# Kernel optimization log

Hardware: AMD Instinct MI355X
Metric: run time of the kernel (lower is better)

Reference implementation:

```python
import jax, jax.numpy as jnp
import numpy as np

H = 1024       # hidden_size
NH = 16        # num_heads
HD = H // NH   # head_dim
I = 4096       # intermediate_size
EPS = 1e-6


def setup_inputs() -> dict:
    key = jax.random.key(0)
    ks = jax.random.split(key, 10)
    s = 0.02
    return {
        "hidden_states": jax.random.normal(ks[0], (8, 1025, H), jnp.float32),
        "qkv_w": jax.random.normal(ks[1], (3 * H, H), jnp.float32) * s,
        "qkv_b": jnp.zeros((3 * H,), jnp.float32),
        "proj_w": jax.random.normal(ks[2], (H, H), jnp.float32) * s,
        "proj_b": jnp.zeros((H,), jnp.float32),
        "fc1_w": jax.random.normal(ks[3], (I, H), jnp.float32) * s,
        "fc1_b": jnp.zeros((I,), jnp.float32),
        "fc2_w": jax.random.normal(ks[4], (H, I), jnp.float32) * s,
        "fc2_b": jnp.zeros((H,), jnp.float32),
        "norm1_w": jnp.ones((H,), jnp.float32),
        "norm1_b": jnp.zeros((H,), jnp.float32),
        "norm2_w": jnp.ones((H,), jnp.float32),
        "norm2_b": jnp.zeros((H,), jnp.float32),
        "ls1": jnp.ones((H,), jnp.float32),
        "ls2": jnp.ones((H,), jnp.float32),
    }


def _layer_norm(x, w, b):
    mu = jnp.mean(x, axis=-1, keepdims=True)
    var = jnp.mean(jnp.square(x - mu), axis=-1, keepdims=True)
    return (x - mu) * jax.lax.rsqrt(var + EPS) * w + b


def _attention(x, qkv_w, qkv_b, proj_w, proj_b):
    B, N, _ = x.shape
    qkv = x @ qkv_w.T + qkv_b                       # [B,N,3H]
    qkv = qkv.reshape(B, N, 3, NH, HD)
    q, k, v = qkv[:, :, 0], qkv[:, :, 1], qkv[:, :, 2]  # [B,N,NH,HD]
    scale = HD ** -0.5
    scores = jnp.einsum("bqhd,bkhd->bhqk", q, k) * scale
    attn = jax.nn.softmax(scores, axis=-1)
    out = jnp.einsum("bhqk,bkhd->bqhd", attn, v).reshape(B, N, H)
    return out @ proj_w.T + proj_b


def _mlp(x, fc1_w, fc1_b, fc2_w, fc2_b):
    h = jax.nn.gelu(x @ fc1_w.T + fc1_b, approximate=False)
    return h @ fc2_w.T + fc2_b


def reference(hidden_states, qkv_w, qkv_b, proj_w, proj_b, fc1_w, fc1_b,
              fc2_w, fc2_b, norm1_w, norm1_b, norm2_w, norm2_b, ls1, ls2):
    x = hidden_states
    x = x + ls1 * _attention(_layer_norm(x, norm1_w, norm1_b),
                             qkv_w, qkv_b, proj_w, proj_b)
    x = x + ls2 * _mlp(_layer_norm(x, norm2_w, norm2_b),
                       fc1_w, fc1_b, fc2_w, fc2_b)
    return x
```

## Files before the change

### kernel.cpp

```cpp
#include <hip/hip_runtime.h>
#include <cstdint>
#include <cstddef>

typedef __bf16 bf16;
typedef __bf16 bf16x8 __attribute__((ext_vector_type(8)));
typedef __bf16 bf16x4 __attribute__((ext_vector_type(4)));
typedef float  floatx4 __attribute__((ext_vector_type(4)));

#define MFMA16(a,b,c) __builtin_amdgcn_mfma_f32_16x16x32_bf16((a),(b),(c),0,0,0)

__device__ __forceinline__ void async_copy16(void* lds, const void* g) {
    __builtin_amdgcn_global_load_lds(
        (const __attribute__((address_space(1))) unsigned int*)g,
        (__attribute__((address_space(3))) unsigned int*)lds,
        16, 0, 0);
}

__global__ __launch_bounds__(256) void cvt_all(const float* __restrict__ s0,
                                               const float* __restrict__ s1,
                                               const float* __restrict__ s2,
                                               const float* __restrict__ s3,
                                               bf16* __restrict__ d0,
                                               bf16* __restrict__ d1,
                                               bf16* __restrict__ d2,
                                               bf16* __restrict__ d3) {
    const int blk = blockIdx.x;
    const float* src; bf16* dst; int base;
    if (blk < 3072)      { src = s0; dst = d0; base = blk; }
    else if (blk < 4096) { src = s1; dst = d1; base = blk - 3072; }
    else if (blk < 8192) { src = s2; dst = d2; base = blk - 4096; }
    else                 { src = s3; dst = d3; base = blk - 8192; }
    const int i = base * 256 + threadIdx.x;
    const float4 v = ((const float4*)src)[i];
    bf16x4 o;
    o[0] = (bf16)v.x; o[1] = (bf16)v.y; o[2] = (bf16)v.z; o[3] = (bf16)v.w;
    ((bf16x4*)dst)[i] = o;
}

__global__ __launch_bounds__(256) void ln_kernel(const float* __restrict__ x,
                                                 const float* __restrict__ w,
                                                 const float* __restrict__ b,
                                                 bf16* __restrict__ out) {
    const int row = blockIdx.x;
    const int t = threadIdx.x;
    const float4 v = ((const float4*)(x + (size_t)row * 1024))[t];
    float s  = v.x + v.y + v.z + v.w;
    float ss = v.x*v.x + v.y*v.y + v.z*v.z + v.w*v.w;
#pragma unroll
    for (int m = 32; m >= 1; m >>= 1) {
        s  += __shfl_xor(s,  m, 64);
        ss += __shfl_xor(ss, m, 64);
    }
    __shared__ float red[8];
    const int wave = t >> 6, lane = t & 63;
    if (lane == 0) { red[wave] = s; red[4 + wave] = ss; }
    __syncthreads();
    s  = red[0] + red[1] + red[2] + red[3];
    ss = red[4] + red[5] + red[6] + red[7];
    const float mean = s * (1.0f / 1024.0f);
    const float var  = ss * (1.0f / 1024.0f) - mean * mean;
    const float inv  = rsqrtf(var + 1e-6f);
    const float4 wv = ((const float4*)w)[t];
    const float4 bv = ((const float4*)b)[t];
    bf16x4 o;
    o[0] = (bf16)((v.x - mean) * inv * wv.x + bv.x);
    o[1] = (bf16)((v.y - mean) * inv * wv.y + bv.y);
    o[2] = (bf16)((v.z - mean) * inv * wv.z + bv.z);
    o[3] = (bf16)((v.w - mean) * inv * wv.w + bv.w);
    *(bf16x4*)(out + (size_t)row * 1024 + t * 4) = o;
}

template <int EPI, bool MSTRIP>
__global__ __launch_bounds__(256, 3) void gemm_bt(
    const bf16* __restrict__ A, const bf16* __restrict__ B,
    const float* __restrict__ bias, void* __restrict__ Cout,
    const float* __restrict__ res, const float* __restrict__ lsv,
    int M, int N, int K, int mt_per) {
    __shared__ bf16 sA[128 * 64];
    __shared__ bf16 sB[128 * 64];
    const int tid  = threadIdx.x;
    const int wave = tid >> 6;
    const int lane = tid & 63;
    const int lrow = lane & 15;
    const int quad = lane >> 4;
    int m0, n0;
    if constexpr (MSTRIP) {
        const int mtile = blockIdx.x * mt_per + blockIdx.y % mt_per;
        const int ntile = blockIdx.y / mt_per;
        m0 = mtile * 128;
        n0 = ntile * 128;
        if (m0 >= M) return;
    } else {
        const int nx   = gridDim.x;
        const int lin  = blockIdx.y * nx + blockIdx.x;
        const int w    = nx >> 3;
        const int xcd  = lin & 7;
        const int slot = lin >> 3;
        const int ntile = xcd * w + (slot % w);
        const int mtile = slot / w;
        m0 = mtile * 128;
        n0 = ntile * 128;
    }
    const int wm = (wave >> 1) * 64;
    const int wn = (wave & 1) * 64;

    floatx4 acc[4][4] = {};

    const int srow  = tid >> 3;
    const int spart = (tid & 7) ^ (srow & 7);
    const bf16* Ag[4];
    const bf16* Bg[4];
#pragma unroll
    for (int c = 0; c < 4; c++) {
        int am = m0 + c * 32 + srow; if (am > M - 1) am = M - 1;
        Ag[c] = A + (size_t)am * K + spart * 8;
        Bg[c] = B + (size_t)(n0 + c * 32 + srow) * K + spart * 8;
    }
    const int sswz = lrow & 7;

    for (int kk = 0; kk < K; kk += 64) {
        __syncthreads();
#pragma unroll
        for (int c = 0; c < 4; c++) {
            async_copy16(&sA[(c * 256 + wave * 64) * 8], Ag[c] + kk);
            async_copy16(&sB[(c * 256 + wave * 64) * 8], Bg[c] + kk);
        }
        __syncthreads();
#pragma unroll
        for (int kq = 0; kq < 2; kq++) {
            const int so = ((kq * 4 + quad) ^ sswz) * 8;
            bf16x8 af[4], bfr[4];
#pragma unroll
            for (int i = 0; i < 4; i++)
                af[i] = *(const bf16x8*)&sA[(wm + i * 16 + lrow) * 64 + so];
#pragma unroll
            for (int j = 0; j < 4; j++)
                bfr[j] = *(const bf16x8*)&sB[(wn + j * 16 + lrow) * 64 + so];
#pragma unroll
            for (int i = 0; i < 4; i++)
#pragma unroll
                for (int j = 0; j < 4; j++)
                    acc[i][j] = MFMA16(af[i], bfr[j], acc[i][j]);
        }
    }

    const int nb = n0 + wn + lrow;
#pragma unroll
    for (int i = 0; i < 4; i++) {
        const int mb = m0 + wm + i * 16 + quad * 4;
#pragma unroll
        for (int r = 0; r < 4; r++) {
            const int m = mb + r;
            if (m < M) {
#pragma unroll
                for (int j = 0; j < 4; j++) {
                    const int n = nb + j * 16;
                    float v = acc[i][j][r] + bias[n];
                    if constexpr (EPI == 0) {
                        ((bf16*)Cout)[(size_t)m * N + n] = (bf16)v;
                    } else if constexpr (EPI == 2) {
                        const float s_ = v * (0.7978845608f + 0.0356774081f * v * v);
                        const float e2s = __builtin_amdgcn_exp2f(2.8853900817779268f * s_);
                        const float g = v * (1.0f - __builtin_amdgcn_rcpf(1.0f + e2s));
                        ((bf16*)Cout)[(size_t)m * N + n] = (bf16)g;
                    } else {
                        ((float*)Cout)[(size_t)m * N + n] =
                            res[(size_t)m * N + n] + lsv[n] * v;
                    }
                }
            }
        }
    }
}

__global__ __launch_bounds__(256) void transpose_v(const bf16* __restrict__ qkv,
                                                   bf16* __restrict__ vt) {
    const int tt = blockIdx.x;
    const int bh = blockIdx.y;
    const int b = bh >> 4, h = bh & 15;
    __shared__ bf16 tile[64][72];
    const int t = threadIdx.x;
    const int tok0 = tt * 64;
#pragma unroll
    for (int i = 0; i < 4; i++) {
        const int idx4 = i * 256 + t;
        const int tl = idx4 >> 4;
        const int d4 = (idx4 & 15) * 4;
        const int tok = tok0 + tl;
        bf16x4 val;
        val[0] = (bf16)0.0f; val[1] = (bf16)0.0f; val[2] = (bf16)0.0f; val[3] = (bf16)0.0f;
        if (tok <= 1024) {
            val = *(const bf16x4*)(qkv + ((size_t)(b * 1025 + tok)) * 3072 + 2048 + h * 64 + d4);
        }
        tile[d4 + 0][tl] = val[0];
        tile[d4 + 1][tl] = val[1];
        tile[d4 + 2][tl] = val[2];
        tile[d4 + 3][tl] = val[3];
    }
    __syncthreads();
#pragma unroll
    for (int i = 0; i < 4; i++) {
        const int idx4 = i * 256 + t;
        const int d = idx4 >> 4;
        const int t4 = (idx4 & 15) * 4;
        bf16x4 o;
        o[0] = tile[d][t4 + 0]; o[1] = tile[d][t4 + 1];
        o[2] = tile[d][t4 + 2]; o[3] = tile[d][t4 + 3];
        *(bf16x4*)(vt + ((size_t)bh * 64 + d) * 1152 + tok0 + t4) = o;
    }
}

__global__ __launch_bounds__(256, 4) void attn_kernel(const bf16* __restrict__ qkv,
                                                      const bf16* __restrict__ vt,
                                                      bf16* __restrict__ o_out) {
    const int qt = blockIdx.x;
    const int bh = blockIdx.y;
    const int b = bh >> 4, h = bh & 15;
    __shared__ bf16 sK[2 * 64 * 32];
    __shared__ bf16 sV[2 * 64 * 32];
    __shared__ bf16 sQP[4 * 16 * 72];
    const int tid = threadIdx.x, wave = tid >> 6, lane = tid & 63;
    const int lrow = lane & 15, quad = lane >> 4, lko = quad * 8;
    const float cexp = 0.18033688011112042f;
    const size_t row0 = (size_t)b * 1025;

#pragma unroll
    for (int i = 0; i < 2; i++) {
        const int g = i * 256 + tid;
        const int ks = g >> 8, rr = (g >> 2) & 63, p = g & 3;
        int qrow = qt * 64 + rr; if (qrow > 1024) qrow = 1024;
        async_copy16(&sQP[(i * 256 + wave * 64) * 8],
                     qkv + (row0 + qrow) * 3072 + h * 64 + ks * 32 + p * 8);
    }
    __syncthreads();
    bf16x8 qf[2];
    qf[0] = *(const bf16x8*)&sQP[(wave * 16 + lrow) * 32 + lko];
    qf[1] = *(const bf16x8*)&sQP[2048 + (wave * 16 + lrow) * 32 + lko];
#pragma unroll
    for (int i = 0; i < 8; i++) {
        qf[0][i] = (bf16)((float)qf[0][i] * cexp);
        qf[1][i] = (bf16)((float)qf[1][i] * cexp);
    }
    bf16x8 ones;
#pragma unroll
    for (int i = 0; i < 8; i++) ones[i] = (bf16)1.0f;

    floatx4 o[4] = {};
    floatx4 ol = {};
    bf16* pw = &sQP[wave * (16 * 72)];

    for (int ktile = 0; ktile < 17; ++ktile) {
        const int kt0 = ktile * 64;
        __syncthreads();
#pragma unroll
        for (int i = 0; i < 2; i++) {
            const int g = i * 256 + tid;
            const int ks = g >> 8, tok = (g >> 2) & 63, p = g & 3;
            int krow = kt0 + tok; if (krow > 1024) krow = 1024;
            async_copy16(&sK[(i * 256 + wave * 64) * 8],
                         qkv + (row0 + krow) * 3072 + 1024 + h * 64 + ks * 32 + p * 8);
        }
#pragma unroll
        for (int i = 0; i < 2; i++) {
            const int g = i * 256 + tid;
            const int kc = g >> 8, d = (g >> 2) & 63, p = g & 3;
            async_copy16(&sV[(i * 256 + wave * 64) * 8],
                         vt + ((size_t)bh * 64 + d) * 1152 + kt0 + kc * 32 + p * 8);
        }
        __syncthreads();

        const bool lastTile = (ktile == 16);
#pragma unroll
        for (int nt = 0; nt < 4; nt++) {
            bf16x8 k0 = *(const bf16x8*)&sK[(nt * 16 + lrow) * 32 + lko];
            bf16x8 k1 = *(const bf16x8*)&sK[2048 + (nt * 16 + lrow) * 32 + lko];
            floatx4 z = {};
            z = MFMA16(k0, qf[0], z);
            z = MFMA16(k1, qf[1], z);
            bf16x4 pb;
#pragma unroll
            for (int r = 0; r < 4; r++) {
                float p = __builtin_amdgcn_exp2f(z[r]);
                if (lastTile) {
                    const int ktok = kt0 + nt * 16 + quad * 4 + r;
                    p = (ktok <= 1024) ? p : 0.0f;
                }
                pb[r] = (bf16)p;
            }
            *(bf16x4*)&pw[lrow * 72 + nt * 16 + quad * 4] = pb;
        }
#pragma unroll
        for (int ks = 0; ks < 2; ks++) {
            bf16x8 pa = *(const bf16x8*)&pw[lrow * 72 + ks * 32 + lko];
#pragma unroll
            for (int j = 0; j < 4; j++) {
                bf16x8 vb = *(const bf16x8*)&sV[ks * 2048 + (j * 16 + lrow) * 32 + lko];
                o[j] = MFMA16(pa, vb, o[j]);
            }
            ol = MFMA16(pa, ones, ol);
        }
    }

#pragma unroll
    for (int r = 0; r < 4; r++) {
        const int q = qt * 64 + wave * 16 + quad * 4 + r;
        if (q <= 1024) {
            const float inv = 1.0f / ol[r];
            const size_t orow = (row0 + q) * 1024 + h * 64;
#pragma unroll
            for (int j = 0; j < 4; j++)
                o_out[orow + j * 16 + lrow] = (bf16)(o[j][r] * inv);
        }
    }
}

extern "C" void kernel_launch(void* const* d_in, const int* in_sizes, int n_in,
                              void* d_out, int out_size, void* d_ws, size_t ws_size,
                              hipStream_t stream) {
    const float* x      = (const float*)d_in[0];
    const float* qkv_w  = (const float*)d_in[1];
    const float* qkv_b  = (const float*)d_in[2];
    const float* proj_w = (const float*)d_in[3];
    const float* proj_b = (const float*)d_in[4];
    const float* fc1_w  = (const float*)d_in[5];
    const float* fc1_b  = (const float*)d_in[6];
    const float* fc2_w  = (const float*)d_in[7];
    const float* fc2_b  = (const float*)d_in[8];
    const float* n1w    = (const float*)d_in[9];
    const float* n1b    = (const float*)d_in[10];
    const float* n2w    = (const float*)d_in[11];
    const float* n2b    = (const float*)d_in[12];
    const float* ls1    = (const float*)d_in[13];
    const float* ls2    = (const float*)d_in[14];

    char* ws = (char*)d_ws;
    bf16*  wqkv  = (bf16*)(ws + 0);
    bf16*  wproj = (bf16*)(ws + 6291456);
    bf16*  wfc1  = (bf16*)(ws + 8388608);
    bf16*  wfc2  = (bf16*)(ws + 16777216);
    bf16*  vt    = (bf16*)(ws + 25165824);
    bf16*  attnO = (bf16*)(ws + 44040192);
    float* x1    = (float*)(ws + 60833792);
    bf16*  lnbuf = (bf16*)(ws + 94420992);
    bf16*  big   = (bf16*)(ws + 111214592);

    const int M = 8200;

    cvt_all<<<12288, 256, 0, stream>>>(qkv_w, proj_w, fc1_w, fc2_w,
                                       wqkv, wproj, wfc1, wfc2);

    ln_kernel<<<M, 256, 0, stream>>>(x, n1w, n1b, lnbuf);
    gemm_bt<0, false><<<dim3(24, 65), 256, 0, stream>>>(lnbuf, wqkv, qkv_b, (void*)big,
                                                        nullptr, nullptr, M, 3072, 1024, 0);
    transpose_v<<<dim3(17, 128), 256, 0, stream>>>(big, vt);
    attn_kernel<<<dim3(17, 128), 256, 0, stream>>>(big, vt, attnO);
    gemm_bt<1, true><<<dim3(8, 72), 256, 0, stream>>>(attnO, wproj, proj_b, (void*)x1,
                                                      x, ls1, M, 1024, 1024, 9);
    ln_kernel<<<M, 256, 0, stream>>>(x1, n2w, n2b, lnbuf);
    gemm_bt<2, false><<<dim3(32, 65), 256, 0, stream>>>(lnbuf, wfc1, fc1_b, (void*)big,
                                                        nullptr, nullptr, M, 4096, 1024, 0);
    gemm_bt<3, true><<<dim3(8, 72), 256, 0, stream>>>(big, wfc2, fc2_b, d_out,
                                                      x1, ls2, M, 1024, 4096, 9);
}
```

Baseline: 505.8 us.

## Split-K the projection and fc2 GEMMs with atomic accumulation into pre-initialized output

The two N=1024 GEMMs (attention projection and fc2) are split along K into two halves via gridDim.z, doubling the number of blocks to improve occupancy across the GPU. A new init_out kernel first writes residual + ls*bias into the output, and each K-slice then atomically adds ls*partial into it. This trades extra atomic traffic and an extra elementwise pass over the output for more parallelism in the under-filled GEMMs, and makes the floating-point summation order nondeterministic.

```diff
diff --git a/kernel.cpp b/kernel.cpp
--- a/kernel.cpp
+++ b/kernel.cpp
@@ -37,6 +37,21 @@
     ((bf16x4*)dst)[i] = o;
 }
 
+__global__ __launch_bounds__(256) void init_out(const float* __restrict__ res,
+                                                const float* __restrict__ lsv,
+                                                const float* __restrict__ bias,
+                                                float* __restrict__ out) {
+    const size_t i = (size_t)blockIdx.x * 256 + threadIdx.x;
+    const int n4 = (int)(i & 255);
+    const float4 r = ((const float4*)res)[i];
+    const float4 l = ((const float4*)lsv)[n4];
+    const float4 b = ((const float4*)bias)[n4];
+    float4 o;
+    o.x = r.x + l.x * b.x; o.y = r.y + l.y * b.y;
+    o.z = r.z + l.z * b.z; o.w = r.w + l.w * b.w;
+    ((float4*)out)[i] = o;
+}
+
 __global__ __launch_bounds__(256) void ln_kernel(const float* __restrict__ x,
                                                  const float* __restrict__ w,
                                                  const float* __restrict__ b,
@@ -74,7 +89,7 @@
 __global__ __launch_bounds__(256, 3) void gemm_bt(
     const bf16* __restrict__ A, const bf16* __restrict__ B,
     const float* __restrict__ bias, void* __restrict__ Cout,
-    const float* __restrict__ res, const float* __restrict__ lsv,
+    const float* __restrict__ lsv,
     int M, int N, int K, int mt_per) {
     __shared__ bf16 sA[128 * 64];
     __shared__ bf16 sB[128 * 64];
@@ -101,6 +116,8 @@
         m0 = mtile * 128;
         n0 = ntile * 128;
     }
+    const int kLen = K / gridDim.z;
+    const int k0   = blockIdx.z * kLen;
     const int wm = (wave >> 1) * 64;
     const int wn = (wave & 1) * 64;
 
@@ -118,7 +135,7 @@
     }
     const int sswz = lrow & 7;
 
-    for (int kk = 0; kk < K; kk += 64) {
+    for (int kk = k0; kk < k0 + kLen; kk += 64) {
         __syncthreads();
 #pragma unroll
         for (int c = 0; c < 4; c++) {
@@ -155,17 +172,18 @@
 #pragma unroll
                 for (int j = 0; j < 4; j++) {
                     const int n = nb + j * 16;
-                    float v = acc[i][j][r] + bias[n];
                     if constexpr (EPI == 0) {
+                        const float v = acc[i][j][r] + bias[n];
                         ((bf16*)Cout)[(size_t)m * N + n] = (bf16)v;
                     } else if constexpr (EPI == 2) {
+                        const float v = acc[i][j][r] + bias[n];
                         const float s_ = v * (0.7978845608f + 0.0356774081f * v * v);
                         const float e2s = __builtin_amdgcn_exp2f(2.8853900817779268f * s_);
                         const float g = v * (1.0f - __builtin_amdgcn_rcpf(1.0f + e2s));
                         ((bf16*)Cout)[(size_t)m * N + n] = (bf16)g;
                     } else {
-                        ((float*)Cout)[(size_t)m * N + n] =
-                            res[(size_t)m * N + n] + lsv[n] * v;
+                        unsafeAtomicAdd(&((float*)Cout)[(size_t)m * N + n],
+                                        lsv[n] * acc[i][j][r]);
                     }
                 }
             }
@@ -351,14 +369,16 @@
 
     ln_kernel<<<M, 256, 0, stream>>>(x, n1w, n1b, lnbuf);
     gemm_bt<0, false><<<dim3(24, 65), 256, 0, stream>>>(lnbuf, wqkv, qkv_b, (void*)big,
-                                                        nullptr, nullptr, M, 3072, 1024, 0);
+                                                        nullptr, M, 3072, 1024, 0);
     transpose_v<<<dim3(17, 128), 256, 0, stream>>>(big, vt);
     attn_kernel<<<dim3(17, 128), 256, 0, stream>>>(big, vt, attnO);
-    gemm_bt<1, true><<<dim3(8, 72), 256, 0, stream>>>(attnO, wproj, proj_b, (void*)x1,
-                                                      x, ls1, M, 1024, 1024, 9);
+    init_out<<<M, 256, 0, stream>>>(x, ls1, proj_b, x1);
+    gemm_bt<1, true><<<dim3(8, 72, 2), 256, 0, stream>>>(attnO, wproj, nullptr, (void*)x1,
+                                                         ls1, M, 1024, 1024, 9);
     ln_kernel<<<M, 256, 0, stream>>>(x1, n2w, n2b, lnbuf);
     gemm_bt<2, false><<<dim3(32, 65), 256, 0, stream>>>(lnbuf, wfc1, fc1_b, (void*)big,
-                                                        nullptr, nullptr, M, 4096, 1024, 0);
-    gemm_bt<3, true><<<dim3(8, 72), 256, 0, stream>>>(big, wfc2, fc2_b, d_out,
-                                                      x1, ls2, M, 1024, 4096, 9);
-}
+                                                        nullptr, M, 4096, 1024, 0);
+    init_out<<<M, 256, 0, stream>>>(x1, ls2, fc2_b, (float*)d_out);
+    gemm_bt<1, true><<<dim3(8, 72, 2), 256, 0, stream>>>(big, wfc2, nullptr, d_out,
+                                                         ls2, M, 1024, 4096, 9);
+}
```

Result: slower. 620.1 us (+22.6%).

## Double-buffer LDS tiles in GEMM and attention to overlap loads with MFMA

Applied to the files above, without the earlier changes.

The GEMM now uses two LDS buffers with a K-step of 32 and a paired-row tile layout. The next tile is prefetched asynchronously while MFMAs run on the current one, cutting the loop to one barrier per iteration. The attention kernel gets the same treatment for its K and V tiles, with an extra barrier so the Q staging area can be reused for P. Occupancy hints are retuned (GEMM 4 blocks, attention 3) to fit the larger LDS footprint. In exchange, the GEMM has half the work per barrier and a new LDS layout that may cause bank conflicts.

```diff
diff --git a/kernel.cpp b/kernel.cpp
--- a/kernel.cpp
+++ b/kernel.cpp
@@ -71,13 +71,13 @@
 }
 
 template <int EPI, bool MSTRIP>
-__global__ __launch_bounds__(256, 3) void gemm_bt(
+__global__ __launch_bounds__(256, 4) void gemm_bt(
     const bf16* __restrict__ A, const bf16* __restrict__ B,
     const float* __restrict__ bias, void* __restrict__ Cout,
     const float* __restrict__ res, const float* __restrict__ lsv,
     int M, int N, int K, int mt_per) {
-    __shared__ bf16 sA[128 * 64];
-    __shared__ bf16 sB[128 * 64];
+    __shared__ bf16 sA[2][4096];
+    __shared__ bf16 sB[2][4096];
     const int tid  = threadIdx.x;
     const int wave = tid >> 6;
     const int lane = tid & 63;
@@ -106,42 +106,51 @@
 
     floatx4 acc[4][4] = {};
 
-    const int srow  = tid >> 3;
-    const int spart = (tid & 7) ^ (srow & 7);
-    const bf16* Ag[4];
-    const bf16* Bg[4];
-#pragma unroll
-    for (int c = 0; c < 4; c++) {
-        int am = m0 + c * 32 + srow; if (am > M - 1) am = M - 1;
-        Ag[c] = A + (size_t)am * K + spart * 8;
-        Bg[c] = B + (size_t)(n0 + c * 32 + srow) * K + spart * 8;
-    }
-    const int sswz = lrow & 7;
-
-    for (int kk = 0; kk < K; kk += 64) {
+    const int part = tid & 3;
+    int mA0 = m0 + 2 * (tid >> 3) + ((tid >> 2) & 1);
+    int mA1 = mA0 + 64;
+    if (mA0 > M - 1) mA0 = M - 1;
+    if (mA1 > M - 1) mA1 = M - 1;
+    const int nB0 = n0 + 2 * (tid >> 3) + ((tid >> 2) & 1);
+    const bf16* AgC0 = A + (size_t)mA0 * K + part * 8;
+    const bf16* AgC1 = A + (size_t)mA1 * K + part * 8;
+    const bf16* BgC0 = B + (size_t)nB0 * K + part * 8;
+    const bf16* BgC1 = B + (size_t)(nB0 + 64) * K + part * 8;
+    const int ldsOff0 = wave * 512;
+    const int ldsOff1 = 2048 + wave * 512;
+
+    const int niter = K / 32;
+    async_copy16(&sA[0][ldsOff0], AgC0);
+    async_copy16(&sA[0][ldsOff1], AgC1);
+    async_copy16(&sB[0][ldsOff0], BgC0);
+    async_copy16(&sB[0][ldsOff1], BgC1);
+
+    const int fbase = (lrow & 1) * 32 + quad * 8;
+    int cur = 0;
+    for (int it = 0; it < niter; ++it) {
         __syncthreads();
-#pragma unroll
-        for (int c = 0; c < 4; c++) {
-            async_copy16(&sA[(c * 256 + wave * 64) * 8], Ag[c] + kk);
-            async_copy16(&sB[(c * 256 + wave * 64) * 8], Bg[c] + kk);
-        }
-        __syncthreads();
-#pragma unroll
-        for (int kq = 0; kq < 2; kq++) {
-            const int so = ((kq * 4 + quad) ^ sswz) * 8;
-            bf16x8 af[4], bfr[4];
-#pragma unroll
-            for (int i = 0; i < 4; i++)
-                af[i] = *(const bf16x8*)&sA[(wm + i * 16 + lrow) * 64 + so];
+        if (it + 1 < niter) {
+            const int kk = (it + 1) * 32;
+            bf16* a = sA[cur ^ 1]; bf16* bb = sB[cur ^ 1];
+            async_copy16(&a[ldsOff0],  AgC0 + kk);
+            async_copy16(&a[ldsOff1],  AgC1 + kk);
+            async_copy16(&bb[ldsOff0], BgC0 + kk);
+            async_copy16(&bb[ldsOff1], BgC1 + kk);
+        }
+        const bf16* a = sA[cur]; const bf16* bb = sB[cur];
+        bf16x8 af[4], bfr[4];
+#pragma unroll
+        for (int i = 0; i < 4; i++)
+            af[i] = *(const bf16x8*)&a[((wm >> 1) + i * 8 + (lrow >> 1)) * 64 + fbase];
+#pragma unroll
+        for (int j = 0; j < 4; j++)
+            bfr[j] = *(const bf16x8*)&bb[((wn >> 1) + j * 8 + (lrow >> 1)) * 64 + fbase];
+#pragma unroll
+        for (int i = 0; i < 4; i++)
 #pragma unroll
             for (int j = 0; j < 4; j++)
-                bfr[j] = *(const bf16x8*)&sB[(wn + j * 16 + lrow) * 64 + so];
-#pragma unroll
-            for (int i = 0; i < 4; i++)
-#pragma unroll
-                for (int j = 0; j < 4; j++)
-                    acc[i][j] = MFMA16(af[i], bfr[j], acc[i][j]);
-        }
+                acc[i][j] = MFMA16(af[i], bfr[j], acc[i][j]);
+        cur ^= 1;
     }
 
     const int nb = n0 + wn + lrow;
@@ -155,7 +164,7 @@
 #pragma unroll
                 for (int j = 0; j < 4; j++) {
                     const int n = nb + j * 16;
-                    float v = acc[i][j][r] + bias[n];
+                    const float v = acc[i][j][r] + bias[n];
                     if constexpr (EPI == 0) {
                         ((bf16*)Cout)[(size_t)m * N + n] = (bf16)v;
                     } else if constexpr (EPI == 2) {
@@ -210,15 +219,15 @@
     }
 }
 
-__global__ __launch_bounds__(256, 4) void attn_kernel(const bf16* __restrict__ qkv,
+__global__ __launch_bounds__(256, 3) void attn_kernel(const bf16* __restrict__ qkv,
                                                       const bf16* __restrict__ vt,
                                                       bf16* __restrict__ o_out) {
     const int qt = blockIdx.x;
     const int bh = blockIdx.y;
     const int b = bh >> 4, h = bh & 15;
-    __shared__ bf16 sK[2 * 64 * 32];
-    __shared__ bf16 sV[2 * 64 * 32];
-    __shared__ bf16 sQP[4 * 16 * 72];
+    __shared__ bf16 sK[2][4096];
+    __shared__ bf16 sV[2][4096];
+    __shared__ bf16 sQP[4608];
     const int tid = threadIdx.x, wave = tid >> 6, lane = tid & 63;
     const int lrow = lane & 15, quad = lane >> 4, lko = quad * 8;
     const float cexp = 0.18033688011112042f;
@@ -241,39 +250,68 @@
         qf[0][i] = (bf16)((float)qf[0][i] * cexp);
         qf[1][i] = (bf16)((float)qf[1][i] * cexp);
     }
+    __syncthreads();
+
+    const int kgs = tid >> 8, p_ = tid & 3;
+    (void)kgs; (void)p_;
+
+    {
+#pragma unroll
+        for (int i = 0; i < 2; i++) {
+            const int g = i * 256 + tid;
+            const int ks = g >> 8, tok = (g >> 2) & 63, p = g & 3;
+            int krow = tok; if (krow > 1024) krow = 1024;
+            async_copy16(&sK[0][(i * 256 + wave * 64) * 8],
+                         qkv + (row0 + krow) * 3072 + 1024 + h * 64 + ks * 32 + p * 8);
+        }
+#pragma unroll
+        for (int i = 0; i < 2; i++) {
+            const int g = i * 256 + tid;
+            const int kc = g >> 8, d = (g >> 2) & 63, p = g & 3;
+            async_copy16(&sV[0][(i * 256 + wave * 64) * 8],
+                         vt + ((size_t)bh * 64 + d) * 1152 + kc * 32 + p * 8);
+        }
+    }
+
     bf16x8 ones;
 #pragma unroll
     for (int i = 0; i < 8; i++) ones[i] = (bf16)1.0f;
 
     floatx4 o[4] = {};
     floatx4 ol = {};
-    bf16* pw = &sQP[wave * (16 * 72)];
-
+    bf16* pw = &sQP[wave * 1152];
+
+    int cur = 0;
     for (int ktile = 0; ktile < 17; ++ktile) {
         const int kt0 = ktile * 64;
         __syncthreads();
-#pragma unroll
-        for (int i = 0; i < 2; i++) {
-            const int g = i * 256 + tid;
-            const int ks = g >> 8, tok = (g >> 2) & 63, p = g & 3;
-            int krow = kt0 + tok; if (krow > 1024) krow = 1024;
-            async_copy16(&sK[(i * 256 + wave * 64) * 8],
-                         qkv + (row0 + krow) * 3072 + 1024 + h * 64 + ks * 32 + p * 8);
-        }
-#pragma unroll
-        for (int i = 0; i < 2; i++) {
-            const int g = i * 256 + tid;
-            const int kc = g >> 8, d = (g >> 2) & 63, p = g & 3;
-            async_copy16(&sV[(i * 256 + wave * 64) * 8],
-                         vt + ((size_t)bh * 64 + d) * 1152 + kt0 + kc * 32 + p * 8);
-        }
-        __syncthreads();
+        if (ktile < 16) {
+            const int nt0 = kt0 + 64;
+            bf16* kb = sK[cur ^ 1]; bf16* vb_ = sV[cur ^ 1];
+#pragma unroll
+            for (int i = 0; i < 2; i++) {
+                const int g = i * 256 + tid;
+                const int ks = g >> 8, tok = (g >> 2) & 63, p = g & 3;
+                int krow = nt0 + tok; if (krow > 1024) krow = 1024;
+                async_copy16(&kb[(i * 256 + wave * 64) * 8],
+                             qkv + (row0 + krow) * 3072 + 1024 + h * 64 + ks * 32 + p * 8);
+            }
+#pragma unroll
+            for (int i = 0; i < 2; i++) {
+                const int g = i * 256 + tid;
+                const int kc = g >> 8, d = (g >> 2) & 63, p = g & 3;
+                async_copy16(&vb_[(i * 256 + wave * 64) * 8],
+                             vt + ((size_t)bh * 64 + d) * 1152 + nt0 + kc * 32 + p * 8);
+            }
+        }
+        const bf16* kbuf = sK[cur];
+        const bf16* vbuf = sV[cur];
 
         const bool lastTile = (ktile == 16);
 #pragma unroll
         for (int nt = 0; nt < 4; nt++) {
-            bf16x8 k0 = *(const bf16x8*)&sK[(nt * 16 + lrow) * 32 + lko];
-            bf16x8 k1 = *(const bf16x8*)&sK[2048 + (nt * 16 + lrow) * 32 + lko];
+            bf16x8 k0 = *(const bf16x8*)&kbuf[(nt * 16 + lrow) * 32 + lko];
+            bf16x8 k1 = *(const bf16x8*)&kbuf[2048 + (nt * 16 + lrow) * 32 + lko];
             floatx4 z = {};
             z = MFMA16(k0, qf[0], z);
             z = MFMA16(k1, qf[1], z);
@@ -294,11 +332,12 @@
             bf16x8 pa = *(const bf16x8*)&pw[lrow * 72 + ks * 32 + lko];
 #pragma unroll
             for (int j = 0; j < 4; j++) {
-                bf16x8 vb = *(const bf16x8*)&sV[ks * 2048 + (j * 16 + lrow) * 32 + lko];
+                bf16x8 vb = *(const bf16x8*)&vbuf[ks * 2048 + (j * 16 + lrow) * 32 + lko];
                 o[j] = MFMA16(pa, vb, o[j]);
             }
             ol = MFMA16(pa, ones, ol);
         }
+        cur ^= 1;
     }
 
 #pragma unroll
@@ -359,6 +398,6 @@
     ln_kernel<<<M, 256, 0, stream>>>(x1, n2w, n2b, lnbuf);
     gemm_bt<2, false><<<dim3(32, 65), 256, 0, stream>>>(lnbuf, wfc1, fc1_b, (void*)big,
                                                         nullptr, nullptr, M, 4096, 1024, 0);
-    gemm_bt<3, true><<<dim3(8, 72), 256, 0, stream>>>(big, wfc2, fc2_b, d_out,
+    gemm_bt<1, true><<<dim3(8, 72), 256, 0, stream>>>(big, wfc2, fc2_b, d_out,
                                                       x1, ls2, M, 1024, 4096, 9);
 }
```

New measurement: 543.2 us. 1.07x slower.
